# Kernel optimization log

Measured on AMD Instinct MI355X. Metric: run time of the kernel, lower is better.

Reference implementation:

```python
import jax, jax.numpy as jnp
import numpy as np

B, S, H = 256, 1, 2048
Q_SIZE = 4096        # num_heads * head_dim = 32 * 128
QKV = 4 * H          # expected_linear_qkv = 8192
K_SZ = 4             # conv kernel size
C = 32               # ssm channels
WSCALE = 0.02


def setup_inputs() -> dict:
    key = jax.random.key(0)
    ks = jax.random.split(key, 13)
    return {
        "hidden_states": jax.random.normal(ks[0], (B, S, H), jnp.float32),
        "W_qkv": jax.random.normal(ks[1], (QKV, H), jnp.float32) * WSCALE,
        "b_qkv": jax.random.normal(ks[2], (QKV,), jnp.float32) * WSCALE,
        "W_gate": jax.random.normal(ks[3], (2 * H, H), jnp.float32) * WSCALE,
        "W_alpha": jax.random.normal(ks[4], (C, H), jnp.float32) * WSCALE,
        "W_beta": jax.random.normal(ks[5], (C, H), jnp.float32) * WSCALE,
        "W_out": jax.random.normal(ks[6], (H, 2 * H), jnp.float32) * WSCALE,
        "ssm_state_a": jax.random.normal(ks[7], (C,), jnp.float32),
        "ssm_dt_bias": jax.random.normal(ks[8], (C,), jnp.float32),
        "ssm_norm_weight": jnp.ones((128,), jnp.float32),
        "conv_kernel": jax.random.normal(ks[9], (QKV, K_SZ), jnp.float32) * WSCALE,
        "ssm_state": jax.random.normal(ks[10], (B, C), jnp.float32),
        "conv_state": jax.random.normal(ks[11], (B, K_SZ, QKV), jnp.float32),
    }


def reference(hidden_states, W_qkv, b_qkv, W_gate, W_alpha, W_beta, W_out,
              ssm_state_a, ssm_dt_bias, ssm_norm_weight, conv_kernel,
              ssm_state, conv_state):
    bsz = hidden_states.shape[0]
    # qkv projection (decode: only last token matters downstream)
    qkv = jnp.einsum('bsh,dh->bsd', hidden_states, W_qkv) + b_qkv  # [B,S,4H]
    mixed_qkv = qkv[:, -1, :].astype(jnp.float32)                  # [B,4H]
    hidden_last = hidden_states[:, -1, :]                          # [B,H]

    # roll conv state and append current token, then causal conv1d step
    cs = jnp.concatenate([conv_state[:, 1:, :], mixed_qkv[:, None, :]], axis=1)  # [B,K,4H]
    conv_out = jnp.einsum('bkd,dk->bd', cs, conv_kernel)           # [B,4H]

    target_size = conv_out.shape[-1] - Q_SIZE                      # 2H = 4096
    k_size = target_size // 2                                      # 2048
    core_base = conv_out[:, Q_SIZE:]                               # [B,2H]
    k_proj = core_base[:, :k_size]
    v_proj = core_base[:, k_size:]

    # alpha/beta gating of the SSM state
    a = hidden_last @ W_alpha.T                                    # [B,C]
    b = hidden_last @ W_beta.T                                     # [B,C]
    g = -jnp.exp(ssm_state_a)[None, :] * jax.nn.softplus(a + ssm_dt_bias[None, :])
    beta = jax.nn.sigmoid(b)

    group_width = k_size // C                                      # 64
    v_group = v_proj[:, :group_width * C].reshape(bsz, C, group_width).mean(-1)
    k_group = k_proj[:, :group_width * C].reshape(bsz, C, group_width).mean(-1)

    new_state = jnp.exp(g) * ssm_state + beta * v_group            # [B,C]
    state_signal = new_state * jax.nn.sigmoid(k_group)             # [B,C]

    repeat_factor = target_size // C                               # 128
    expanded = jnp.repeat(state_signal, repeat_factor, axis=-1)[:, :target_size]

    core = core_base + expanded
    core = core * jax.lax.rsqrt(jnp.mean(core * core, axis=-1, keepdims=True) + 1e-6)
    gate = jax.nn.sigmoid(hidden_last @ W_gate.T).astype(jnp.float32)
    core = core * gate * jnp.mean(ssm_norm_weight)
    core = core.astype(hidden_states.dtype)

    out = (core @ W_out.T)[:, None, :]                             # [B,1,H]
    return out
```

## Files before the change

### kernel.cpp

```cpp
#include <hip/hip_runtime.h>
#include <hip/hip_bf16.h>
#include <stdint.h>

#define BSZ 256
#define NQ 4096
#define N1 8320
#define K1 2048
#define N3 2048
#define K3 4096

typedef __attribute__((ext_vector_type(8))) short bf16x8;
typedef __attribute__((ext_vector_type(4))) float f32x4;

__device__ __forceinline__ unsigned short f2bf(float f) {
  union { float f; unsigned u; } v; v.f = f;
  unsigned r = v.u + 0x7fffu + ((v.u >> 16) & 1u);
  return (unsigned short)(r >> 16);
}

__device__ __forceinline__ bf16x8 pack8(float4 a, float4 b) {
  union { bf16x8 v; unsigned short u[8]; } o;
  o.u[0] = f2bf(a.x); o.u[1] = f2bf(a.y); o.u[2] = f2bf(a.z); o.u[3] = f2bf(a.w);
  o.u[4] = f2bf(b.x); o.u[5] = f2bf(b.y); o.u[6] = f2bf(b.z); o.u[7] = f2bf(b.w);
  return o.v;
}

__device__ __forceinline__ void gload_lds16(const void* g, void* lds_uniform) {
  __builtin_amdgcn_global_load_lds(
      (const __attribute__((address_space(1))) unsigned int*)g,
      (__attribute__((address_space(3))) unsigned int*)lds_uniform, 16, 0, 0);
}

__global__ __launch_bounds__(256) void cvt_kernel(const float* __restrict__ x,
                                                  unsigned short* __restrict__ y) {
  int i = (blockIdx.x * 256 + threadIdx.x) * 8;
  float4 a = *(const float4*)(x + i);
  float4 b = *(const float4*)(x + i + 4);
  ushort4 o0 = { f2bf(a.x), f2bf(a.y), f2bf(a.z), f2bf(a.w) };
  ushort4 o1 = { f2bf(b.x), f2bf(b.y), f2bf(b.z), f2bf(b.w) };
  *(ushort4*)(y + i) = o0;
  *(ushort4*)(y + i + 4) = o1;
}


__global__ __launch_bounds__(256, 4) void gemm1_kernel(
    const unsigned short* __restrict__ A16,
    const float* __restrict__ Wqkv, const float* __restrict__ Wgate,
    const float* __restrict__ Walpha, const float* __restrict__ Wbeta,
    float* __restrict__ P) {
  __shared__ __align__(16) unsigned short sA[128 * 64];
  __shared__ __align__(16) float sB[32 * 64];
  const int tid = threadIdx.x, lane = tid & 63, wv = tid >> 6;
  const int wr = wv >> 1, wc = wv & 1, l15 = lane & 15;
  const int rt = blockIdx.x * 128;
  const int n0 = blockIdx.y * 32;
  const int kb = blockIdx.z * 1024;

  const char* aS[4]; char* aD[4];
#pragma unroll
  for (int t = 0; t < 4; t++) {
    int s = wv * 4 + t;
    int m = 8 * s + (lane >> 3);
    int c = (lane & 7) ^ ((lane >> 3) & 7);
    aS[t] = (const char*)(A16 + (size_t)(rt + m) * K1 + kb) + c * 16;
    aD[t] = (char*)sA + s * 1024;
  }
  const char* bS[2]; char* bD[2];
#pragma unroll
  for (int t = 0; t < 2; t++) {
    int s = wv * 2 + t;
    int n = 4 * s + (lane >> 4);
    int c = (lane & 15) ^ (n & 15);
    int ng = n0 + n;
    const float* base;
    if (ng < 4096)       base = Wqkv  + (size_t)(4096 + ng) * K1;
    else if (ng < 8192)  base = Wgate + (size_t)(ng - 4096) * K1;
    else if (ng < 8224)  base = Walpha + (size_t)(ng - 8192) * K1;
    else if (ng < 8256)  base = Wbeta + (size_t)(ng - 8224) * K1;
    else                 base = Walpha;
    bS[t] = (const char*)(base + kb) + c * 16;
    bD[t] = (char*)sB + s * 1024;
  }

  f32x4 acc[4];
#pragma unroll
  for (int i = 0; i < 4; i++) { f32x4 z = {0.f, 0.f, 0.f, 0.f}; acc[i] = z; }

  for (int it = 0; it < 16; it++) {
    __syncthreads();
#pragma unroll
    for (int t = 0; t < 4; t++) gload_lds16(aS[t] + it * 128, aD[t]);
#pragma unroll
    for (int t = 0; t < 2; t++) gload_lds16(bS[t] + it * 256, bD[t]);
    __syncthreads();
#pragma unroll
    for (int ks2 = 0; ks2 < 2; ks2++) {
      int nr = wc * 16 + l15;
      int c0 = ks2 * 8 + (lane >> 4) * 2;
      float4 b0 = *(const float4*)((const char*)sB + nr * 256 + ((c0 ^ (nr & 15)) * 16));
      float4 b1 = *(const float4*)((const char*)sB + nr * 256 + (((c0 + 1) ^ (nr & 15)) * 16));
      bf16x8 bF = pack8(b0, b1);
#pragma unroll
      for (int i = 0; i < 4; i++) {
        int m = wr * 64 + i * 16 + l15;
        int cA = ks2 * 4 + (lane >> 4);
        bf16x8 aF = *(const bf16x8*)((const char*)sA + m * 128 + ((cA ^ (m & 7)) * 16));
        acc[i] = __builtin_amdgcn_mfma_f32_16x16x32_bf16(aF, bF, acc[i], 0, 0, 0);
      }
    }
  }

  float* Pz = P + (size_t)blockIdx.z * ((size_t)BSZ * N1);
#pragma unroll
  for (int i = 0; i < 4; i++) {
    int row = rt + wr * 64 + i * 16 + (lane >> 4) * 4;
    int col = n0 + wc * 16 + l15;
#pragma unroll
    for (int r = 0; r < 4; r++)
      Pz[(size_t)(row + r) * N1 + col] = acc[i][r];
  }
}

__global__ __launch_bounds__(512) void fuse_kernel(
    const float* __restrict__ P,
    const float* __restrict__ bqkv,
    const float* __restrict__ ck,
    const float* __restrict__ cstate,
    const float* __restrict__ ssa,
    const float* __restrict__ dtb,
    const float* __restrict__ nw,
    const float* __restrict__ sstate,
    unsigned short* __restrict__ C16) {
  __shared__ __align__(16) float cb[4096];
  __shared__ float gsum[64];
  __shared__ float ssl[32];
  __shared__ float red[16];
  const int b = blockIdx.x, tid = threadIdx.x;
  const int lane = tid & 63, wv = tid >> 6;
  const float* P0 = P + (size_t)b * N1;
  const float* P1 = P + (size_t)(BSZ + b) * N1;

  if (wv == 0) {
    float m = nw[lane] + nw[lane + 64];
#pragma unroll
    for (int off = 32; off; off >>= 1) m += __shfl_down(m, off, 64);
    if (lane == 0) red[8] = m * (1.f / 128.f);
  }

#pragma unroll
  for (int it = 0; it < 2; it++) {
    int j = (it * 512 + tid) * 4;
    float4 q0 = *(const float4*)(P0 + j);
    float4 q1 = *(const float4*)(P1 + j);
    float4 bq = *(const float4*)(bqkv + NQ + j);
    float mqx = q0.x + q1.x + bq.x, mqy = q0.y + q1.y + bq.y;
    float mqz = q0.z + q1.z + bq.z, mqw = q0.w + q1.w + bq.w;
    const float* csb = cstate + (size_t)b * 4 * 8192 + NQ + j;
    float4 c1 = *(const float4*)(csb + 8192);
    float4 c2 = *(const float4*)(csb + 16384);
    float4 c3 = *(const float4*)(csb + 24576);
    float4 k0v = *(const float4*)(ck + (size_t)(NQ + j) * 4);
    float4 k1v = *(const float4*)(ck + (size_t)(NQ + j + 1) * 4);
    float4 k2v = *(const float4*)(ck + (size_t)(NQ + j + 2) * 4);
    float4 k3v = *(const float4*)(ck + (size_t)(NQ + j + 3) * 4);
    float4 cbv;
    cbv.x = c1.x * k0v.x + c2.x * k0v.y + c3.x * k0v.z + mqx * k0v.w;
    cbv.y = c1.y * k1v.x + c2.y * k1v.y + c3.y * k1v.z + mqy * k1v.w;
    cbv.z = c1.z * k2v.x + c2.z * k2v.y + c3.z * k2v.z + mqz * k2v.w;
    cbv.w = c1.w * k3v.x + c2.w * k3v.y + c3.w * k3v.z + mqw * k3v.w;
    *(float4*)(cb + j) = cbv;
    float s = cbv.x + cbv.y + cbv.z + cbv.w;
    s += __shfl_xor(s, 1, 64); s += __shfl_xor(s, 2, 64);
    s += __shfl_xor(s, 4, 64); s += __shfl_xor(s, 8, 64);
    if ((lane & 15) == 0) gsum[(it * 512 + tid) >> 4] = s;
  }
  __syncthreads();

  if (tid < 32) {
    float a  = P0[8192 + tid] + P1[8192 + tid];
    float bc = P0[8224 + tid] + P1[8224 + tid];
    float kg = gsum[tid] * (1.f / 64.f);
    float vg = gsum[32 + tid] * (1.f / 64.f);
    float x = a + dtb[tid];
    float sp = fmaxf(x, 0.f) + log1pf(expf(-fabsf(x)));
    float g = -expf(ssa[tid]) * sp;
    float beta = 1.f / (1.f + expf(-bc));
    float ns = expf(g) * sstate[b * 32 + tid] + beta * vg;
    ssl[tid] = ns / (1.f + expf(-kg));
  }
  __syncthreads();

  float sq = 0.f;
  float4 c1r[2];
#pragma unroll
  for (int it = 0; it < 2; it++) {
    int j = (it * 512 + tid) * 4;
    float4 v = *(const float4*)(cb + j);
    float sv = ssl[j >> 7];
    v.x += sv; v.y += sv; v.z += sv; v.w += sv;
    c1r[it] = v;
    sq += v.x * v.x + v.y * v.y + v.z * v.z + v.w * v.w;
  }
#pragma unroll
  for (int off = 32; off; off >>= 1) sq += __shfl_down(sq, off, 64);
  if (lane == 0) red[wv] = sq;
  __syncthreads();
  if (tid == 0) {
    float t = red[0] + red[1] + red[2] + red[3] + red[4] + red[5] + red[6] + red[7];
    red[9] = rsqrtf(t * (1.f / 4096.f) + 1e-6f);
  }
  __syncthreads();
  float rms = red[9], mwv = red[8];

#pragma unroll
  for (int it = 0; it < 2; it++) {
    int j = (it * 512 + tid) * 4;
    float4 g0x = *(const float4*)(P0 + NQ + j);
    float4 g1x = *(const float4*)(P1 + NQ + j);
    float4 v = c1r[it];
    float ox = v.x * rms * mwv / (1.f + expf(-(g0x.x + g1x.x)));
    float oy = v.y * rms * mwv / (1.f + expf(-(g0x.y + g1x.y)));
    float oz = v.z * rms * mwv / (1.f + expf(-(g0x.z + g1x.z)));
    float ow = v.w * rms * mwv / (1.f + expf(-(g0x.w + g1x.w)));
    ushort4 u = { f2bf(ox), f2bf(oy), f2bf(oz), f2bf(ow) };
    *(ushort4*)(C16 + (size_t)b * 4096 + j) = u;
  }
}

__global__ __launch_bounds__(256, 4) void gemm3_kernel(
    const unsigned short* __restrict__ A16,
    const float* __restrict__ Wout,
    float* __restrict__ OP) {
  __shared__ __align__(16) unsigned short sA[128 * 64];
  __shared__ __align__(16) float sB[32 * 64];
  const int tid = threadIdx.x, lane = tid & 63, wv = tid >> 6;
  const int wr = wv >> 1, wc = wv & 1, l15 = lane & 15;
  const int rt = blockIdx.x * 128;
  const int n0 = blockIdx.y * 32;
  const int kb = blockIdx.z * 512;

  const char* aS[4]; char* aD[4];
#pragma unroll
  for (int t = 0; t < 4; t++) {
    int s = wv * 4 + t;
    int m = 8 * s + (lane >> 3);
    int c = (lane & 7) ^ ((lane >> 3) & 7);
    aS[t] = (const char*)(A16 + (size_t)(rt + m) * K3 + kb) + c * 16;
    aD[t] = (char*)sA + s * 1024;
  }
  const char* bS[2]; char* bD[2];
#pragma unroll
  for (int t = 0; t < 2; t++) {
    int s = wv * 2 + t;
    int n = 4 * s + (lane >> 4);
    int c = (lane & 15) ^ (n & 15);
    bS[t] = (const char*)(Wout + (size_t)(n0 + n) * K3 + kb) + c * 16;
    bD[t] = (char*)sB + s * 1024;
  }

  f32x4 acc[4];
#pragma unroll
  for (int i = 0; i < 4; i++) { f32x4 z = {0.f, 0.f, 0.f, 0.f}; acc[i] = z; }

  for (int it = 0; it < 8; it++) {
    __syncthreads();
#pragma unroll
    for (int t = 0; t < 4; t++) gload_lds16(aS[t] + it * 128, aD[t]);
#pragma unroll
    for (int t = 0; t < 2; t++) gload_lds16(bS[t] + it * 256, bD[t]);
    __syncthreads();
#pragma unroll
    for (int ks2 = 0; ks2 < 2; ks2++) {
      int nr = wc * 16 + l15;
      int c0 = ks2 * 8 + (lane >> 4) * 2;
      float4 b0 = *(const float4*)((const char*)sB + nr * 256 + ((c0 ^ (nr & 15)) * 16));
      float4 b1 = *(const float4*)((const char*)sB + nr * 256 + (((c0 + 1) ^ (nr & 15)) * 16));
      bf16x8 bF = pack8(b0, b1);
#pragma unroll
      for (int i = 0; i < 4; i++) {
        int m = wr * 64 + i * 16 + l15;
        int cA = ks2 * 4 + (lane >> 4);
        bf16x8 aF = *(const bf16x8*)((const char*)sA + m * 128 + ((cA ^ (m & 7)) * 16));
        acc[i] = __builtin_amdgcn_mfma_f32_16x16x32_bf16(aF, bF, acc[i], 0, 0, 0);
      }
    }
  }

  float* Oz = OP + (size_t)blockIdx.z * ((size_t)BSZ * N3);
#pragma unroll
  for (int i = 0; i < 4; i++) {
    int row = rt + wr * 64 + i * 16 + (lane >> 4) * 4;
    int col = n0 + wc * 16 + l15;
#pragma unroll
    for (int r = 0; r < 4; r++)
      Oz[(size_t)(row + r) * N3 + col] = acc[i][r];
  }
}

__global__ __launch_bounds__(256) void reduce_kernel(const float* __restrict__ OP,
                                                     float* __restrict__ out) {
  int i = (blockIdx.x * 256 + threadIdx.x) * 4;
  float4 s = *(const float4*)(OP + i);
#pragma unroll
  for (int z = 1; z < 8; z++) {
    float4 v = *(const float4*)(OP + (size_t)z * BSZ * N3 + i);
    s.x += v.x; s.y += v.y; s.z += v.z; s.w += v.w;
  }
  *(float4*)(out + i) = s;
}

extern "C" void kernel_launch(void* const* d_in, const int* in_sizes, int n_in,
                              void* d_out, int out_size, void* d_ws, size_t ws_size,
                              hipStream_t stream) {
  const float* hidden = (const float*)d_in[0];
  const float* Wqkv   = (const float*)d_in[1];
  const float* bqkv   = (const float*)d_in[2];
  const float* Wgate  = (const float*)d_in[3];
  const float* Walpha = (const float*)d_in[4];
  const float* Wbeta  = (const float*)d_in[5];
  const float* Wout   = (const float*)d_in[6];
  const float* ssa    = (const float*)d_in[7];
  const float* dtb    = (const float*)d_in[8];
  const float* nw     = (const float*)d_in[9];
  const float* ck     = (const float*)d_in[10];
  const float* sstate = (const float*)d_in[11];
  const float* cstate = (const float*)d_in[12];
  float* out = (float*)d_out;

  char* ws = (char*)d_ws;
  unsigned short* A16 = (unsigned short*)ws;
  float* P   = (float*)(ws + (1 << 20));
  unsigned short* C16 = (unsigned short*)(ws + (1 << 20) + 17039360);
  float* OP  = (float*)(ws + (1 << 20) + 17039360 + (2 << 20));

  cvt_kernel<<<256, 256, 0, stream>>>(hidden, A16);
  gemm1_kernel<<<dim3(2, 260, 2), 256, 0, stream>>>(A16, Wqkv, Wgate, Walpha, Wbeta, P);
  fuse_kernel<<<256, 512, 0, stream>>>(P, bqkv, ck, cstate, ssa, dtb, nw, sstate, C16);
  gemm3_kernel<<<dim3(2, 64, 8), 256, 0, stream>>>(C16, Wout, OP);
  reduce_kernel<<<512, 256, 0, stream>>>(OP, out);
}
```

Before: 231.4 us.

## Double-buffer LDS tiles in both GEMMs and cut split-K partitions

After: 232.5 us. Within noise of the previous version (+0.5%).

```diff
diff --git a/kernel.cpp b/kernel.cpp
--- a/kernel.cpp
+++ b/kernel.cpp
@@ -8,6 +8,7 @@
 #define K1 2048
 #define N3 2048
 #define K3 4096
+#define Z3 4
 
 typedef __attribute__((ext_vector_type(8))) short bf16x8;
 typedef __attribute__((ext_vector_type(4))) float f32x4;
@@ -43,18 +44,17 @@
 }
 
 
-__global__ __launch_bounds__(256, 4) void gemm1_kernel(
+__global__ __launch_bounds__(256, 3) void gemm1_kernel(
     const unsigned short* __restrict__ A16,
     const float* __restrict__ Wqkv, const float* __restrict__ Wgate,
     const float* __restrict__ Walpha, const float* __restrict__ Wbeta,
     float* __restrict__ P) {
-  __shared__ __align__(16) unsigned short sA[128 * 64];
-  __shared__ __align__(16) float sB[32 * 64];
+  __shared__ __align__(16) unsigned short sA[2][128 * 64];
+  __shared__ __align__(16) float sB[2][32 * 64];
   const int tid = threadIdx.x, lane = tid & 63, wv = tid >> 6;
   const int wr = wv >> 1, wc = wv & 1, l15 = lane & 15;
   const int rt = blockIdx.x * 128;
   const int n0 = blockIdx.y * 32;
-  const int kb = blockIdx.z * 1024;
 
   const char* aS[4]; char* aD[4];
 #pragma unroll
@@ -62,8 +62,8 @@
     int s = wv * 4 + t;
     int m = 8 * s + (lane >> 3);
     int c = (lane & 7) ^ ((lane >> 3) & 7);
-    aS[t] = (const char*)(A16 + (size_t)(rt + m) * K1 + kb) + c * 16;
-    aD[t] = (char*)sA + s * 1024;
+    aS[t] = (const char*)(A16 + (size_t)(rt + m) * K1) + c * 16;
+    aD[t] = (char*)(&sA[0][0]) + s * 1024;
   }
   const char* bS[2]; char* bD[2];
 #pragma unroll
@@ -78,46 +78,59 @@
     else if (ng < 8224)  base = Walpha + (size_t)(ng - 8192) * K1;
     else if (ng < 8256)  base = Wbeta + (size_t)(ng - 8224) * K1;
     else                 base = Walpha;
-    bS[t] = (const char*)(base + kb) + c * 16;
-    bD[t] = (char*)sB + s * 1024;
+    bS[t] = (const char*)base + c * 16;
+    bD[t] = (char*)(&sB[0][0]) + s * 1024;
   }
 
   f32x4 acc[4];
 #pragma unroll
   for (int i = 0; i < 4; i++) { f32x4 z = {0.f, 0.f, 0.f, 0.f}; acc[i] = z; }
 
-  for (int it = 0; it < 16; it++) {
-    __syncthreads();
-#pragma unroll
-    for (int t = 0; t < 4; t++) gload_lds16(aS[t] + it * 128, aD[t]);
-#pragma unroll
-    for (int t = 0; t < 2; t++) gload_lds16(bS[t] + it * 256, bD[t]);
-    __syncthreads();
+#pragma unroll
+  for (int t = 0; t < 4; t++) gload_lds16(aS[t], aD[t]);
+#pragma unroll
+  for (int t = 0; t < 2; t++) gload_lds16(bS[t], bD[t]);
+  __syncthreads();
+
+  int cur = 0;
+  for (int it = 0; it < 32; it++) {
+    if (it < 31) {
+#pragma unroll
+      for (int t = 0; t < 4; t++)
+        gload_lds16(aS[t] + (it + 1) * 128, aD[t] + (cur ^ 1) * 16384);
+#pragma unroll
+      for (int t = 0; t < 2; t++)
+        gload_lds16(bS[t] + (it + 1) * 256, bD[t] + (cur ^ 1) * 8192);
+    }
+    __builtin_amdgcn_sched_barrier(0);
+    const char* sAb = (const char*)sA + cur * 16384;
+    const char* sBb = (const char*)sB + cur * 8192;
 #pragma unroll
     for (int ks2 = 0; ks2 < 2; ks2++) {
       int nr = wc * 16 + l15;
       int c0 = ks2 * 8 + (lane >> 4) * 2;
-      float4 b0 = *(const float4*)((const char*)sB + nr * 256 + ((c0 ^ (nr & 15)) * 16));
-      float4 b1 = *(const float4*)((const char*)sB + nr * 256 + (((c0 + 1) ^ (nr & 15)) * 16));
+      float4 b0 = *(const float4*)(sBb + nr * 256 + ((c0 ^ (nr & 15)) * 16));
+      float4 b1 = *(const float4*)(sBb + nr * 256 + (((c0 + 1) ^ (nr & 15)) * 16));
       bf16x8 bF = pack8(b0, b1);
 #pragma unroll
       for (int i = 0; i < 4; i++) {
         int m = wr * 64 + i * 16 + l15;
         int cA = ks2 * 4 + (lane >> 4);
-        bf16x8 aF = *(const bf16x8*)((const char*)sA + m * 128 + ((cA ^ (m & 7)) * 16));
+        bf16x8 aF = *(const bf16x8*)(sAb + m * 128 + ((cA ^ (m & 7)) * 16));
         acc[i] = __builtin_amdgcn_mfma_f32_16x16x32_bf16(aF, bF, acc[i], 0, 0, 0);
       }
     }
-  }
-
-  float* Pz = P + (size_t)blockIdx.z * ((size_t)BSZ * N1);
+    __syncthreads();
+    cur ^= 1;
+  }
+
 #pragma unroll
   for (int i = 0; i < 4; i++) {
     int row = rt + wr * 64 + i * 16 + (lane >> 4) * 4;
     int col = n0 + wc * 16 + l15;
 #pragma unroll
     for (int r = 0; r < 4; r++)
-      Pz[(size_t)(row + r) * N1 + col] = acc[i][r];
+      P[(size_t)(row + r) * N1 + col] = acc[i][r];
   }
 }
 
@@ -138,7 +151,6 @@
   const int b = blockIdx.x, tid = threadIdx.x;
   const int lane = tid & 63, wv = tid >> 6;
   const float* P0 = P + (size_t)b * N1;
-  const float* P1 = P + (size_t)(BSZ + b) * N1;
 
   if (wv == 0) {
     float m = nw[lane] + nw[lane + 64];
@@ -151,10 +163,9 @@
   for (int it = 0; it < 2; it++) {
     int j = (it * 512 + tid) * 4;
     float4 q0 = *(const float4*)(P0 + j);
-    float4 q1 = *(const float4*)(P1 + j);
     float4 bq = *(const float4*)(bqkv + NQ + j);
-    float mqx = q0.x + q1.x + bq.x, mqy = q0.y + q1.y + bq.y;
-    float mqz = q0.z + q1.z + bq.z, mqw = q0.w + q1.w + bq.w;
+    float mqx = q0.x + bq.x, mqy = q0.y + bq.y;
+    float mqz = q0.z + bq.z, mqw = q0.w + bq.w;
     const float* csb = cstate + (size_t)b * 4 * 8192 + NQ + j;
     float4 c1 = *(const float4*)(csb + 8192);
     float4 c2 = *(const float4*)(csb + 16384);
@@ -177,8 +188,8 @@
   __syncthreads();
 
   if (tid < 32) {
-    float a  = P0[8192 + tid] + P1[8192 + tid];
-    float bc = P0[8224 + tid] + P1[8224 + tid];
+    float a  = P0[8192 + tid];
+    float bc = P0[8224 + tid];
     float kg = gsum[tid] * (1.f / 64.f);
     float vg = gsum[32 + tid] * (1.f / 64.f);
     float x = a + dtb[tid];
@@ -216,28 +227,27 @@
   for (int it = 0; it < 2; it++) {
     int j = (it * 512 + tid) * 4;
     float4 g0x = *(const float4*)(P0 + NQ + j);
-    float4 g1x = *(const float4*)(P1 + NQ + j);
     float4 v = c1r[it];
-    float ox = v.x * rms * mwv / (1.f + expf(-(g0x.x + g1x.x)));
-    float oy = v.y * rms * mwv / (1.f + expf(-(g0x.y + g1x.y)));
-    float oz = v.z * rms * mwv / (1.f + expf(-(g0x.z + g1x.z)));
-    float ow = v.w * rms * mwv / (1.f + expf(-(g0x.w + g1x.w)));
+    float ox = v.x * rms * mwv / (1.f + expf(-g0x.x));
+    float oy = v.y * rms * mwv / (1.f + expf(-g0x.y));
+    float oz = v.z * rms * mwv / (1.f + expf(-g0x.z));
+    float ow = v.w * rms * mwv / (1.f + expf(-g0x.w));
     ushort4 u = { f2bf(ox), f2bf(oy), f2bf(oz), f2bf(ow) };
     *(ushort4*)(C16 + (size_t)b * 4096 + j) = u;
   }
 }
 
-__global__ __launch_bounds__(256, 4) void gemm3_kernel(
+__global__ __launch_bounds__(256, 3) void gemm3_kernel(
     const unsigned short* __restrict__ A16,
     const float* __restrict__ Wout,
     float* __restrict__ OP) {
-  __shared__ __align__(16) unsigned short sA[128 * 64];
-  __shared__ __align__(16) float sB[32 * 64];
+  __shared__ __align__(16) unsigned short sA[2][128 * 64];
+  __shared__ __align__(16) float sB[2][32 * 64];
   const int tid = threadIdx.x, lane = tid & 63, wv = tid >> 6;
   const int wr = wv >> 1, wc = wv & 1, l15 = lane & 15;
   const int rt = blockIdx.x * 128;
   const int n0 = blockIdx.y * 32;
-  const int kb = blockIdx.z * 512;
+  const int kb = blockIdx.z * 1024;
 
   const char* aS[4]; char* aD[4];
 #pragma unroll
@@ -246,7 +256,7 @@
     int m = 8 * s + (lane >> 3);
     int c = (lane & 7) ^ ((lane >> 3) & 7);
     aS[t] = (const char*)(A16 + (size_t)(rt + m) * K3 + kb) + c * 16;
-    aD[t] = (char*)sA + s * 1024;
+    aD[t] = (char*)(&sA[0][0]) + s * 1024;
   }
   const char* bS[2]; char* bD[2];
 #pragma unroll
@@ -255,35 +265,49 @@
     int n = 4 * s + (lane >> 4);
     int c = (lane & 15) ^ (n & 15);
     bS[t] = (const char*)(Wout + (size_t)(n0 + n) * K3 + kb) + c * 16;
-    bD[t] = (char*)sB + s * 1024;
+    bD[t] = (char*)(&sB[0][0]) + s * 1024;
   }
 
   f32x4 acc[4];
 #pragma unroll
   for (int i = 0; i < 4; i++) { f32x4 z = {0.f, 0.f, 0.f, 0.f}; acc[i] = z; }
 
-  for (int it = 0; it < 8; it++) {
-    __syncthreads();
-#pragma unroll
-    for (int t = 0; t < 4; t++) gload_lds16(aS[t] + it * 128, aD[t]);
-#pragma unroll
-    for (int t = 0; t < 2; t++) gload_lds16(bS[t] + it * 256, bD[t]);
-    __syncthreads();
+#pragma unroll
+  for (int t = 0; t < 4; t++) gload_lds16(aS[t], aD[t]);
+#pragma unroll
+  for (int t = 0; t < 2; t++) gload_lds16(bS[t], bD[t]);
+  __syncthreads();
+
+  int cur = 0;
+  for (int it = 0; it < 16; it++) {
+    if (it < 15) {
+#pragma unroll
+      for (int t = 0; t < 4; t++)
+        gload_lds16(aS[t] + (it + 1) * 128, aD[t] + (cur ^ 1) * 16384);
+#pragma unroll
+      for (int t = 0; t < 2; t++)
+        gload_lds16(bS[t] + (it + 1) * 256, bD[t] + (cur ^ 1) * 8192);
+    }
+    __builtin_amdgcn_sched_barrier(0);
+    const char* sAb = (const char*)sA + cur * 16384;
+    const char* sBb = (const char*)sB + cur * 8192;
 #pragma unroll
     for (int ks2 = 0; ks2 < 2; ks2++) {
       int nr = wc * 16 + l15;
       int c0 = ks2 * 8 + (lane >> 4) * 2;
-      float4 b0 = *(const float4*)((const char*)sB + nr * 256 + ((c0 ^ (nr & 15)) * 16));
-      float4 b1 = *(const float4*)((const char*)sB + nr * 256 + (((c0 + 1) ^ (nr & 15)) * 16));
+      float4 b0 = *(const float4*)(sBb + nr * 256 + ((c0 ^ (nr & 15)) * 16));
+      float4 b1 = *(const float4*)(sBb + nr * 256 + (((c0 + 1) ^ (nr & 15)) * 16));
       bf16x8 bF = pack8(b0, b1);
 #pragma unroll
       for (int i = 0; i < 4; i++) {
         int m = wr * 64 + i * 16 + l15;
         int cA = ks2 * 4 + (lane >> 4);
-        bf16x8 aF = *(const bf16x8*)((const char*)sA + m * 128 + ((cA ^ (m & 7)) * 16));
+        bf16x8 aF = *(const bf16x8*)(sAb + m * 128 + ((cA ^ (m & 7)) * 16));
         acc[i] = __builtin_amdgcn_mfma_f32_16x16x32_bf16(aF, bF, acc[i], 0, 0, 0);
       }
     }
+    __syncthreads();
+    cur ^= 1;
   }
 
   float* Oz = OP + (size_t)blockIdx.z * ((size_t)BSZ * N3);
@@ -302,7 +326,7 @@
   int i = (blockIdx.x * 256 + threadIdx.x) * 4;
   float4 s = *(const float4*)(OP + i);
 #pragma unroll
-  for (int z = 1; z < 8; z++) {
+  for (int z = 1; z < Z3; z++) {
     float4 v = *(const float4*)(OP + (size_t)z * BSZ * N3 + i);
     s.x += v.x; s.y += v.y; s.z += v.z; s.w += v.w;
   }
@@ -330,12 +354,12 @@
   char* ws = (char*)d_ws;
   unsigned short* A16 = (unsigned short*)ws;
   float* P   = (float*)(ws + (1 << 20));
-  unsigned short* C16 = (unsigned short*)(ws + (1 << 20) + 17039360);
-  float* OP  = (float*)(ws + (1 << 20) + 17039360 + (2 << 20));
+  unsigned short* C16 = (unsigned short*)(ws + (1 << 20) + 8519680);
+  float* OP  = (float*)(ws + (1 << 20) + 8519680 + (2 << 20));
 
   cvt_kernel<<<256, 256, 0, stream>>>(hidden, A16);
-  gemm1_kernel<<<dim3(2, 260, 2), 256, 0, stream>>>(A16, Wqkv, Wgate, Walpha, Wbeta, P);
+  gemm1_kernel<<<dim3(2, 260, 1), 256, 0, stream>>>(A16, Wqkv, Wgate, Walpha, Wbeta, P);
   fuse_kernel<<<256, 512, 0, stream>>>(P, bqkv, ck, cstate, ssa, dtb, nw, sstate, C16);
-  gemm3_kernel<<<dim3(2, 64, 8), 256, 0, stream>>>(C16, Wout, OP);
+  gemm3_kernel<<<dim3(2, 64, Z3), 256, 0, stream>>>(C16, Wout, OP);
   reduce_kernel<<<512, 256, 0, stream>>>(OP, out);
 }
```

## Retile GEMMs to full-batch M tiles with bf16 weight staging and deeper split-K

Applied to the files above, without the earlier changes.

Result: faster. 217.1 us (-6.2%).

```diff
diff --git a/kernel.cpp b/kernel.cpp
--- a/kernel.cpp
+++ b/kernel.cpp
@@ -4,10 +4,13 @@
 
 #define BSZ 256
 #define NQ 4096
-#define N1 8320
 #define K1 2048
 #define N3 2048
 #define K3 4096
+#define Z1 4
+#define Z3 8
+#define ZAB 32
+#define PSTR ((size_t)BSZ * 8192)
 
 typedef __attribute__((ext_vector_type(8))) short bf16x8;
 typedef __attribute__((ext_vector_type(4))) float f32x4;
@@ -19,9 +22,11 @@
 }
 
 __device__ __forceinline__ bf16x8 pack8(float4 a, float4 b) {
-  union { bf16x8 v; unsigned short u[8]; } o;
-  o.u[0] = f2bf(a.x); o.u[1] = f2bf(a.y); o.u[2] = f2bf(a.z); o.u[3] = f2bf(a.w);
-  o.u[4] = f2bf(b.x); o.u[5] = f2bf(b.y); o.u[6] = f2bf(b.z); o.u[7] = f2bf(b.w);
+  union { bf16x8 v; __hip_bfloat162 h[4]; } o;
+  o.h[0] = __float22bfloat162_rn(float2{a.x, a.y});
+  o.h[1] = __float22bfloat162_rn(float2{a.z, a.w});
+  o.h[2] = __float22bfloat162_rn(float2{b.x, b.y});
+  o.h[3] = __float22bfloat162_rn(float2{b.z, b.w});
   return o.v;
 }
 
@@ -42,87 +47,163 @@
   *(ushort4*)(y + i + 4) = o1;
 }
 
-
-__global__ __launch_bounds__(256, 4) void gemm1_kernel(
+__global__ __launch_bounds__(512) void gemm1_kernel(
     const unsigned short* __restrict__ A16,
     const float* __restrict__ Wqkv, const float* __restrict__ Wgate,
     const float* __restrict__ Walpha, const float* __restrict__ Wbeta,
-    float* __restrict__ P) {
-  __shared__ __align__(16) unsigned short sA[128 * 64];
-  __shared__ __align__(16) float sB[32 * 64];
+    float* __restrict__ P,
+    float* __restrict__ Pab) {
+  __shared__ __align__(16) unsigned short sA[256 * 64];
+  __shared__ __align__(16) unsigned short sB[128 * 64];
   const int tid = threadIdx.x, lane = tid & 63, wv = tid >> 6;
-  const int wr = wv >> 1, wc = wv & 1, l15 = lane & 15;
-  const int rt = blockIdx.x * 128;
-  const int n0 = blockIdx.y * 32;
-  const int kb = blockIdx.z * 1024;
-
-  const char* aS[4]; char* aD[4];
-#pragma unroll
-  for (int t = 0; t < 4; t++) {
-    int s = wv * 4 + t;
-    int m = 8 * s + (lane >> 3);
-    int c = (lane & 7) ^ ((lane >> 3) & 7);
-    aS[t] = (const char*)(A16 + (size_t)(rt + m) * K1 + kb) + c * 16;
-    aD[t] = (char*)sA + s * 1024;
-  }
-  const char* bS[2]; char* bD[2];
-#pragma unroll
-  for (int t = 0; t < 2; t++) {
-    int s = wv * 2 + t;
-    int n = 4 * s + (lane >> 4);
-    int c = (lane & 15) ^ (n & 15);
-    int ng = n0 + n;
-    const float* base;
-    if (ng < 4096)       base = Wqkv  + (size_t)(4096 + ng) * K1;
-    else if (ng < 8192)  base = Wgate + (size_t)(ng - 4096) * K1;
-    else if (ng < 8224)  base = Walpha + (size_t)(ng - 8192) * K1;
-    else if (ng < 8256)  base = Wbeta + (size_t)(ng - 8224) * K1;
-    else                 base = Walpha;
-    bS[t] = (const char*)(base + kb) + c * 16;
-    bD[t] = (char*)sB + s * 1024;
-  }
-
-  f32x4 acc[4];
-#pragma unroll
-  for (int i = 0; i < 4; i++) { f32x4 z = {0.f, 0.f, 0.f, 0.f}; acc[i] = z; }
-
-  for (int it = 0; it < 16; it++) {
+  const int l15 = lane & 15, q4 = lane >> 4;
+  const int wm = wv >> 1, wn = wv & 1;
+  const int bx = blockIdx.x;
+
+  if (bx < 256) {
+    const int n0 = (bx & 63) * 128;
+    const int k0 = (bx >> 6) * 512;
+
+    const char* aS[4]; char* aD[4];
+#pragma unroll
+    for (int t = 0; t < 4; t++) {
+      int s = wv * 4 + t;
+      int m = 8 * s + (lane >> 3);
+      int c = (lane & 7) ^ ((lane >> 3) & 7);
+      aS[t] = (const char*)(A16 + (size_t)m * K1 + k0) + c * 16;
+      aD[t] = (char*)sA + s * 1024;
+    }
+    const int r = tid >> 2, qq = tid & 3;
+    const int ng = n0 + r;
+    const float* Bp = (ng < 4096 ? Wqkv + (size_t)(4096 + ng) * K1
+                                 : Wgate + (size_t)(ng - 4096) * K1) + k0 + qq * 16;
+    char* bw0 = (char*)sB + r * 128 + (((2 * qq) ^ (r & 7)) * 16);
+    char* bw1 = (char*)sB + r * 128 + (((2 * qq + 1) ^ (r & 7)) * 16);
+
+    f32x4 acc[4][4];
+#pragma unroll
+    for (int i = 0; i < 4; i++)
+#pragma unroll
+      for (int j = 0; j < 4; j++) { f32x4 z = {0.f,0.f,0.f,0.f}; acc[i][j] = z; }
+
+    float4 br0 = *(const float4*)(Bp);
+    float4 br1 = *(const float4*)(Bp + 4);
+    float4 br2 = *(const float4*)(Bp + 8);
+    float4 br3 = *(const float4*)(Bp + 12);
+
+    for (int it = 0; it < 8; ++it) {
+      __syncthreads();
+#pragma unroll
+      for (int t = 0; t < 4; t++) gload_lds16(aS[t] + it * 128, aD[t]);
+      *(bf16x8*)bw0 = pack8(br0, br1);
+      *(bf16x8*)bw1 = pack8(br2, br3);
+      __syncthreads();
+      if (it < 7) {
+        const float* bp = Bp + (it + 1) * 64;
+        br0 = *(const float4*)(bp);
+        br1 = *(const float4*)(bp + 4);
+        br2 = *(const float4*)(bp + 8);
+        br3 = *(const float4*)(bp + 12);
+      }
+#pragma unroll
+      for (int ks = 0; ks < 2; ks++) {
+        bf16x8 bF[4];
+#pragma unroll
+        for (int j = 0; j < 4; j++) {
+          int row = wn * 64 + j * 16 + l15;
+          bF[j] = *(const bf16x8*)((const char*)sB + row * 128 +
+                                   (((ks * 4 + q4) ^ (row & 7)) * 16));
+        }
+#pragma unroll
+        for (int i = 0; i < 4; i++) {
+          int m = wm * 64 + i * 16 + l15;
+          bf16x8 aF = *(const bf16x8*)((const char*)sA + m * 128 +
+                                       (((ks * 4 + q4) ^ (m & 7)) * 16));
+#pragma unroll
+          for (int j = 0; j < 4; j++)
+            acc[i][j] = __builtin_amdgcn_mfma_f32_16x16x32_bf16(aF, bF[j], acc[i][j], 0, 0, 0);
+        }
+      }
+    }
+
+    float* Pz = P + (size_t)(bx >> 6) * PSTR;
+#pragma unroll
+    for (int i = 0; i < 4; i++)
+#pragma unroll
+      for (int j = 0; j < 4; j++) {
+        int row = wm * 64 + i * 16 + q4 * 4;
+        int col = n0 + wn * 64 + j * 16 + l15;
+#pragma unroll
+        for (int rr = 0; rr < 4; rr++)
+          Pz[(size_t)(row + rr) * 8192 + col] = acc[i][j][rr];
+      }
+  } else {
+    const int iab = bx - 256;
+    const int kk = iab * 64;
+
+    const char* aS[4]; char* aD[4];
+#pragma unroll
+    for (int t = 0; t < 4; t++) {
+      int s = wv * 4 + t;
+      int m = 8 * s + (lane >> 3);
+      int c = (lane & 7) ^ ((lane >> 3) & 7);
+      aS[t] = (const char*)(A16 + (size_t)m * K1 + kk) + c * 16;
+      aD[t] = (char*)sA + s * 1024;
+    }
+    const int r = tid >> 3, e = tid & 7;
+    const float* Bp = (r < 32 ? Walpha + (size_t)r * K1
+                              : Wbeta + (size_t)(r - 32) * K1) + kk + e * 8;
+    float4 br0 = *(const float4*)(Bp);
+    float4 br1 = *(const float4*)(Bp + 4);
+
+#pragma unroll
+    for (int t = 0; t < 4; t++) gload_lds16(aS[t], aD[t]);
+    *(bf16x8*)((char*)sB + r * 128 + ((e ^ (r & 7)) * 16)) = pack8(br0, br1);
     __syncthreads();
-#pragma unroll
-    for (int t = 0; t < 4; t++) gload_lds16(aS[t] + it * 128, aD[t]);
-#pragma unroll
-    for (int t = 0; t < 2; t++) gload_lds16(bS[t] + it * 256, bD[t]);
-    __syncthreads();
-#pragma unroll
-    for (int ks2 = 0; ks2 < 2; ks2++) {
-      int nr = wc * 16 + l15;
-      int c0 = ks2 * 8 + (lane >> 4) * 2;
-      float4 b0 = *(const float4*)((const char*)sB + nr * 256 + ((c0 ^ (nr & 15)) * 16));
-      float4 b1 = *(const float4*)((const char*)sB + nr * 256 + (((c0 + 1) ^ (nr & 15)) * 16));
-      bf16x8 bF = pack8(b0, b1);
+
+    f32x4 acc[4][2];
+#pragma unroll
+    for (int i = 0; i < 4; i++)
+#pragma unroll
+      for (int j = 0; j < 2; j++) { f32x4 z = {0.f,0.f,0.f,0.f}; acc[i][j] = z; }
+
+#pragma unroll
+    for (int ks = 0; ks < 2; ks++) {
+      bf16x8 bF[2];
+#pragma unroll
+      for (int j = 0; j < 2; j++) {
+        int row = wn * 32 + j * 16 + l15;
+        bF[j] = *(const bf16x8*)((const char*)sB + row * 128 +
+                                 (((ks * 4 + q4) ^ (row & 7)) * 16));
+      }
 #pragma unroll
       for (int i = 0; i < 4; i++) {
-        int m = wr * 64 + i * 16 + l15;
-        int cA = ks2 * 4 + (lane >> 4);
-        bf16x8 aF = *(const bf16x8*)((const char*)sA + m * 128 + ((cA ^ (m & 7)) * 16));
-        acc[i] = __builtin_amdgcn_mfma_f32_16x16x32_bf16(aF, bF, acc[i], 0, 0, 0);
-      }
-    }
-  }
-
-  float* Pz = P + (size_t)blockIdx.z * ((size_t)BSZ * N1);
-#pragma unroll
-  for (int i = 0; i < 4; i++) {
-    int row = rt + wr * 64 + i * 16 + (lane >> 4) * 4;
-    int col = n0 + wc * 16 + l15;
-#pragma unroll
-    for (int r = 0; r < 4; r++)
-      Pz[(size_t)(row + r) * N1 + col] = acc[i][r];
+        int m = wm * 64 + i * 16 + l15;
+        bf16x8 aF = *(const bf16x8*)((const char*)sA + m * 128 +
+                                     (((ks * 4 + q4) ^ (m & 7)) * 16));
+#pragma unroll
+        for (int j = 0; j < 2; j++)
+          acc[i][j] = __builtin_amdgcn_mfma_f32_16x16x32_bf16(aF, bF[j], acc[i][j], 0, 0, 0);
+      }
+    }
+
+    float* Pz = Pab + (size_t)iab * (BSZ * 64);
+#pragma unroll
+    for (int i = 0; i < 4; i++)
+#pragma unroll
+      for (int j = 0; j < 2; j++) {
+        int row = wm * 64 + i * 16 + q4 * 4;
+        int col = wn * 32 + j * 16 + l15;
+#pragma unroll
+        for (int rr = 0; rr < 4; rr++)
+          Pz[(size_t)(row + rr) * 64 + col] = acc[i][j][rr];
+      }
   }
 }
 
 __global__ __launch_bounds__(512) void fuse_kernel(
     const float* __restrict__ P,
+    const float* __restrict__ Pab,
     const float* __restrict__ bqkv,
     const float* __restrict__ ck,
     const float* __restrict__ cstate,
@@ -137,8 +218,7 @@
   __shared__ float red[16];
   const int b = blockIdx.x, tid = threadIdx.x;
   const int lane = tid & 63, wv = tid >> 6;
-  const float* P0 = P + (size_t)b * N1;
-  const float* P1 = P + (size_t)(BSZ + b) * N1;
+  const float* P0 = P + (size_t)b * 8192;
 
   if (wv == 0) {
     float m = nw[lane] + nw[lane + 64];
@@ -150,11 +230,15 @@
 #pragma unroll
   for (int it = 0; it < 2; it++) {
     int j = (it * 512 + tid) * 4;
-    float4 q0 = *(const float4*)(P0 + j);
-    float4 q1 = *(const float4*)(P1 + j);
+    float4 p0 = *(const float4*)(P0 + j);
+    float4 p1 = *(const float4*)(P0 + PSTR + j);
+    float4 p2 = *(const float4*)(P0 + 2 * PSTR + j);
+    float4 p3 = *(const float4*)(P0 + 3 * PSTR + j);
     float4 bq = *(const float4*)(bqkv + NQ + j);
-    float mqx = q0.x + q1.x + bq.x, mqy = q0.y + q1.y + bq.y;
-    float mqz = q0.z + q1.z + bq.z, mqw = q0.w + q1.w + bq.w;
+    float mqx = p0.x + p1.x + p2.x + p3.x + bq.x;
+    float mqy = p0.y + p1.y + p2.y + p3.y + bq.y;
+    float mqz = p0.z + p1.z + p2.z + p3.z + bq.z;
+    float mqw = p0.w + p1.w + p2.w + p3.w + bq.w;
     const float* csb = cstate + (size_t)b * 4 * 8192 + NQ + j;
     float4 c1 = *(const float4*)(csb + 8192);
     float4 c2 = *(const float4*)(csb + 16384);
@@ -177,8 +261,13 @@
   __syncthreads();
 
   if (tid < 32) {
-    float a  = P0[8192 + tid] + P1[8192 + tid];
-    float bc = P0[8224 + tid] + P1[8224 + tid];
+    float a = 0.f, bc = 0.f;
+    const float* pa = Pab + (size_t)b * 64 + tid;
+#pragma unroll
+    for (int s = 0; s < ZAB; s++) {
+      a  += pa[(size_t)s * (BSZ * 64)];
+      bc += pa[(size_t)s * (BSZ * 64) + 32];
+    }
     float kg = gsum[tid] * (1.f / 64.f);
     float vg = gsum[32 + tid] * (1.f / 64.f);
     float x = a + dtb[tid];
@@ -215,29 +304,35 @@
 #pragma unroll
   for (int it = 0; it < 2; it++) {
     int j = (it * 512 + tid) * 4;
-    float4 g0x = *(const float4*)(P0 + NQ + j);
-    float4 g1x = *(const float4*)(P1 + NQ + j);
+    float4 g0 = *(const float4*)(P0 + NQ + j);
+    float4 g1 = *(const float4*)(P0 + PSTR + NQ + j);
+    float4 g2 = *(const float4*)(P0 + 2 * PSTR + NQ + j);
+    float4 g3 = *(const float4*)(P0 + 3 * PSTR + NQ + j);
+    float gx = g0.x + g1.x + g2.x + g3.x;
+    float gy = g0.y + g1.y + g2.y + g3.y;
+    float gz = g0.z + g1.z + g2.z + g3.z;
+    float gw = g0.w + g1.w + g2.w + g3.w;
     float4 v = c1r[it];
-    float ox = v.x * rms * mwv / (1.f + expf(-(g0x.x + g1x.x)));
-    float oy = v.y * rms * mwv / (1.f + expf(-(g0x.y + g1x.y)));
-    float oz = v.z * rms * mwv / (1.f + expf(-(g0x.z + g1x.z)));
-    float ow = v.w * rms * mwv / (1.f + expf(-(g0x.w + g1x.w)));
+    float ox = v.x * rms * mwv / (1.f + expf(-gx));
+    float oy = v.y * rms * mwv / (1.f + expf(-gy));
+    float oz = v.z * rms * mwv / (1.f + expf(-gz));
+    float ow = v.w * rms * mwv / (1.f + expf(-gw));
     ushort4 u = { f2bf(ox), f2bf(oy), f2bf(oz), f2bf(ow) };
     *(ushort4*)(C16 + (size_t)b * 4096 + j) = u;
   }
 }
 
-__global__ __launch_bounds__(256, 4) void gemm3_kernel(
+__global__ __launch_bounds__(512) void gemm3_kernel(
     const unsigned short* __restrict__ A16,
     const float* __restrict__ Wout,
     float* __restrict__ OP) {
-  __shared__ __align__(16) unsigned short sA[128 * 64];
-  __shared__ __align__(16) float sB[32 * 64];
+  __shared__ __align__(16) unsigned short sA[256 * 64];
+  __shared__ __align__(16) unsigned short sB[64 * 64];
   const int tid = threadIdx.x, lane = tid & 63, wv = tid >> 6;
-  const int wr = wv >> 1, wc = wv & 1, l15 = lane & 15;
-  const int rt = blockIdx.x * 128;
-  const int n0 = blockIdx.y * 32;
-  const int kb = blockIdx.z * 512;
+  const int l15 = lane & 15, q4 = lane >> 4;
+  const int wm = wv >> 1, wn = wv & 1;
+  const int n0 = (blockIdx.x & 31) * 64;
+  const int k0 = (blockIdx.x >> 5) * 512;
 
   const char* aS[4]; char* aD[4];
 #pragma unroll
@@ -245,56 +340,65 @@
     int s = wv * 4 + t;
     int m = 8 * s + (lane >> 3);
     int c = (lane & 7) ^ ((lane >> 3) & 7);
-    aS[t] = (const char*)(A16 + (size_t)(rt + m) * K3 + kb) + c * 16;
+    aS[t] = (const char*)(A16 + (size_t)m * K3 + k0) + c * 16;
     aD[t] = (char*)sA + s * 1024;
   }
-  const char* bS[2]; char* bD[2];
-#pragma unroll
-  for (int t = 0; t < 2; t++) {
-    int s = wv * 2 + t;
-    int n = 4 * s + (lane >> 4);
-    int c = (lane & 15) ^ (n & 15);
-    bS[t] = (const char*)(Wout + (size_t)(n0 + n) * K3 + kb) + c * 16;
-    bD[t] = (char*)sB + s * 1024;
-  }
-
-  f32x4 acc[4];
-#pragma unroll
-  for (int i = 0; i < 4; i++) { f32x4 z = {0.f, 0.f, 0.f, 0.f}; acc[i] = z; }
-
-  for (int it = 0; it < 8; it++) {
+  const int r = tid >> 3, e = tid & 7;
+  const float* Bp = Wout + (size_t)(n0 + r) * K3 + k0 + e * 8;
+  char* bw = (char*)sB + r * 128 + ((e ^ (r & 7)) * 16);
+
+  f32x4 acc[4][2];
+#pragma unroll
+  for (int i = 0; i < 4; i++)
+#pragma unroll
+    for (int j = 0; j < 2; j++) { f32x4 z = {0.f,0.f,0.f,0.f}; acc[i][j] = z; }
+
+  float4 br0 = *(const float4*)(Bp);
+  float4 br1 = *(const float4*)(Bp + 4);
+
+  for (int it = 0; it < 8; ++it) {
     __syncthreads();
 #pragma unroll
     for (int t = 0; t < 4; t++) gload_lds16(aS[t] + it * 128, aD[t]);
-#pragma unroll
-    for (int t = 0; t < 2; t++) gload_lds16(bS[t] + it * 256, bD[t]);
+    *(bf16x8*)bw = pack8(br0, br1);
     __syncthreads();
-#pragma unroll
-    for (int ks2 = 0; ks2 < 2; ks2++) {
-      int nr = wc * 16 + l15;
-      int c0 = ks2 * 8 + (lane >> 4) * 2;
-      float4 b0 = *(const float4*)((const char*)sB + nr * 256 + ((c0 ^ (nr & 15)) * 16));
-      float4 b1 = *(const float4*)((const char*)sB + nr * 256 + (((c0 + 1) ^ (nr & 15)) * 16));
-      bf16x8 bF = pack8(b0, b1);
+    if (it < 7) {
+      const float* bp = Bp + (it + 1) * 64;
+      br0 = *(const float4*)(bp);
+      br1 = *(const float4*)(bp + 4);
+    }
+#pragma unroll
+    for (int ks = 0; ks < 2; ks++) {
+      bf16x8 bF[2];
+#pragma unroll
+      for (int j = 0; j < 2; j++) {
+        int row = wn * 32 + j * 16 + l15;
+        bF[j] = *(const bf16x8*)((const char*)sB + row * 128 +
+                                 (((ks * 4 + q4) ^ (row & 7)) * 16));
+      }
 #pragma unroll
       for (int i = 0; i < 4; i++) {
-        int m = wr * 64 + i * 16 + l15;
-        int cA = ks2 * 4 + (lane >> 4);
-        bf16x8 aF = *(const bf16x8*)((const char*)sA + m * 128 + ((cA ^ (m & 7)) * 16));
-        acc[i] = __builtin_amdgcn_mfma_f32_16x16x32_bf16(aF, bF, acc[i], 0, 0, 0);
-      }
-    }
-  }
-
-  float* Oz = OP + (size_t)blockIdx.z * ((size_t)BSZ * N3);
-#pragma unroll
-  for (int i = 0; i < 4; i++) {
-    int row = rt + wr * 64 + i * 16 + (lane >> 4) * 4;
-    int col = n0 + wc * 16 + l15;
-#pragma unroll
-    for (int r = 0; r < 4; r++)
-      Oz[(size_t)(row + r) * N3 + col] = acc[i][r];
-  }
+        int m = wm * 64 + i * 16 + l15;
+        bf16x8 aF = *(const bf16x8*)((const char*)sA + m * 128 +
+                                     (((ks * 4 + q4) ^ (m & 7)) * 16));
+#pragma unroll
+        for (int j = 0; j < 2; j++)
+          acc[i][j] = __builtin_amdgcn_mfma_f32_16x16x32_bf16(aF, bF[j], acc[i][j], 0, 0, 0);
+      }
+    }
+  }
+
+  float* Oz = OP + (size_t)(blockIdx.x >> 5) * ((size_t)BSZ * N3);
+#pragma unroll
+  for (int i = 0; i < 4; i++)
+#pragma unroll
+    for (int j = 0; j < 2; j++) {
+      int row = wm * 64 + i * 16 + q4 * 4;
+      int col = n0 + wn * 32 + j * 16 + l15;
+#pragma unroll
+      for (int rr = 0; rr < 4; rr++)
+        Oz[(size_t)(row + rr) * N3 + col] = acc[i][j][rr];
+    }
 }
 
 __global__ __launch_bounds__(256) void reduce_kernel(const float* __restrict__ OP,
@@ -302,7 +406,7 @@
   int i = (blockIdx.x * 256 + threadIdx.x) * 4;
   float4 s = *(const float4*)(OP + i);
 #pragma unroll
-  for (int z = 1; z < 8; z++) {
+  for (int z = 1; z < Z3; z++) {
     float4 v = *(const float4*)(OP + (size_t)z * BSZ * N3 + i);
     s.x += v.x; s.y += v.y; s.z += v.z; s.w += v.w;
   }
@@ -330,12 +434,13 @@
   char* ws = (char*)d_ws;
   unsigned short* A16 = (unsigned short*)ws;
   float* P   = (float*)(ws + (1 << 20));
-  unsigned short* C16 = (unsigned short*)(ws + (1 << 20) + 17039360);
-  float* OP  = (float*)(ws + (1 << 20) + 17039360 + (2 << 20));
+  float* Pab = (float*)(ws + (1 << 20) + (32 << 20));
+  unsigned short* C16 = (unsigned short*)(ws + (35 << 20));
+  float* OP  = P;
 
   cvt_kernel<<<256, 256, 0, stream>>>(hidden, A16);
-  gemm1_kernel<<<dim3(2, 260, 2), 256, 0, stream>>>(A16, Wqkv, Wgate, Walpha, Wbeta, P);
-  fuse_kernel<<<256, 512, 0, stream>>>(P, bqkv, ck, cstate, ssa, dtb, nw, sstate, C16);
-  gemm3_kernel<<<dim3(2, 64, 8), 256, 0, stream>>>(C16, Wout, OP);
+  gemm1_kernel<<<288, 512, 0, stream>>>(A16, Wqkv, Wgate, Walpha, Wbeta, P, Pab);
+  fuse_kernel<<<256, 512, 0, stream>>>(P, Pab, bqkv, ck, cstate, ssa, dtb, nw, sstate, C16);
+  gemm3_kernel<<<256, 512, 0, stream>>>(C16, Wout, OP);
   reduce_kernel<<<512, 256, 0, stream>>>(OP, out);
 }
```
